# Kernel tuning notes

Hardware: AMD Instinct MI355X
Metric: run time of the kernel (lower is better)

The kernel has to match this reference:

```python
import jax, jax.numpy as jnp
import numpy as np

# Static part-graph structure (matches adj_matrix in init_kwargs; torch.nonzero row-major order)
ADJ = np.array([[0,1,0,0,0,0],
                [1,0,1,1,1,1],
                [0,1,0,0,0,0],
                [0,1,0,0,0,0],
                [0,1,0,0,0,0],
                [0,1,0,0,0,0]], dtype=np.int64)
_EDGES = np.argwhere(ADJ)            # [E,2] = (src, dst)
SRC = jnp.asarray(_EDGES[:, 0])
DST = jnp.asarray(_EDGES[:, 1])
NUM_PARTS = 6
# parts 1..4 are upper (use xh[0]), parts 5..6 lower (use xh[1])
HALVES = jnp.array([0, 0, 0, 0, 1, 1])


def setup_inputs() -> dict:
    key = jax.random.key(0)
    ks = jax.random.split(key, 12)
    B, H, W, Cin, h, P = 16, 96, 96, 256, 10, NUM_PARTS
    s = 0.05  # weight scale
    return {
        "p_fea":    jax.random.normal(ks[0], (B, Cin, H, W), jnp.float32),
        "xp_stack": jax.random.normal(ks[1], (P, B, h, H, W), jnp.float32),
        "xh_stack": jax.random.normal(ks[2], (2, B, h, H, W), jnp.float32),
        "w_att":  jax.random.normal(ks[3], (P, h), jnp.float32) * s,      # grouped 1x1 conv (groups=P)
        "b_att":  jnp.zeros((P,), jnp.float32),
        "w_dp_f": jax.random.normal(ks[4], (h, Cin), jnp.float32) * s,    # Part_Dependency: p_fea branch
        "w_dp_x": jax.random.normal(ks[5], (h, h), jnp.float32) * s,      # Part_Dependency: xp branch
        "b_dp":   jnp.zeros((h,), jnp.float32),
        "w_proj": jax.random.normal(ks[6], (P, h, Cin), jnp.float32) * s, # Decomposition proj (per part)
        "b_proj": jnp.zeros((P, h), jnp.float32),
        "w_gate": jax.random.normal(ks[7], (P, 2 * h), jnp.float32) * s,  # Decomposition gate on cat(xh,xp)
        "b_gate": jnp.zeros((P,), jnp.float32),
        "w_upd":  jax.random.normal(ks[8], (P, h, 3 * h), jnp.float32) * s,  # att_Update on cat(xp,xpp,xhp)
        "b_upd":  jnp.zeros((P, h), jnp.float32),
    }


def reference(p_fea, xp_stack, xh_stack, w_att, b_att, w_dp_f, w_dp_x, b_dp,
              w_proj, b_proj, w_gate, b_gate, w_upd, b_upd):
    # xp_stack: [P,B,h,H,W], p_fea: [B,Cin,H,W]
    P = xp_stack.shape[0]

    # grouped 1x1 conv + sigmoid -> per-part attention map [P,B,1,H,W]
    att = jax.nn.sigmoid(jnp.einsum('pbchw,pc->pbhw', xp_stack, w_att)
                         + b_att[:, None, None, None])[:, :, None]

    # Part_Dependency: dp_i = relu(W_f @ p_fea + W_x @ xp_i + b), shared weights -> [P,B,h,H,W]
    dp = jax.nn.relu(jnp.einsum('bchw,dc->bdhw', p_fea, w_dp_f)[None]
                     + jnp.einsum('pbchw,dc->pbdhw', xp_stack, w_dp_x)
                     + b_dp[None, None, :, None, None])

    # Pair_Part_Dependency per edge: sigmoid-gated fusion, then sum-aggregate at dst
    msg = att[SRC] * att[DST] * (dp[SRC] + xp_stack[DST])   # [E,B,h,H,W]
    xpp = jax.ops.segment_sum(msg, DST, num_segments=P)     # [P,B,h,H,W]

    # Decomposition: gate half-body feature onto a projection of p_fea (per-part weights)
    xh_sel = xh_stack[HALVES]                                # [P,B,h,H,W]
    proj = jnp.einsum('bchw,pdc->pbdhw', p_fea, w_proj) + b_proj[:, None, :, None, None]
    gate = jax.nn.sigmoid(jnp.einsum('pbchw,pc->pbhw',
                                     jnp.concatenate([xh_sel, xp_stack], axis=2), w_gate)
                          + b_gate[:, None, None, None])[:, :, None]
    xhp = gate * proj                                        # [P,B,h,H,W]

    # att_Update: residual update from cat(xp, xpp, xhp) via per-part 1x1 conv
    cat3 = jnp.concatenate([xp_stack, xpp, xhp], axis=2)     # [P,B,3h,H,W]
    xp_out = xp_stack + jax.nn.relu(jnp.einsum('pbchw,pdc->pbdhw', cat3, w_upd)
                                    + b_upd[:, None, :, None, None])
    return xp_out, xpp, xhp
```

## Files before the change

### kernel.cpp

```cpp
#include <hip/hip_runtime.h>

#define HWSZ 9216
#define CIN  256
#define NPER 8847360
#define PSTRIDE 1474560
#define IMG_STRIDE 2359296
#define BHW 92160

#define OFF_WATT  18432
#define OFF_BATT  18492
#define OFF_WDPX  18498
#define OFF_BDP   18598
#define OFF_BPROJ 18608
#define OFF_WGATE 18668
#define OFF_BGATE 18788
#define OFF_WUPD  18794
#define OFF_BUPD  20594
#define WS_TOTAL  20654
#define A_OFF_U16 41472
#define A_ELEMS   20480

typedef __attribute__((ext_vector_type(8))) short short8;
typedef __attribute__((ext_vector_type(4))) float f32x4;
typedef __attribute__((ext_vector_type(2))) float f32x2;

#define SS     66
#define L_S    0
#define L_DP1  4620
#define L_S1   5280
#define L_SA   5940
#define L_ATT  6008
#define L_GATE 6392
#define L_TOT  6776

static __device__ __forceinline__ unsigned short f2b(float f) {
  union { float f; unsigned int i; } v; v.f = f;
  unsigned int u = v.i;
  return (unsigned short)((u + 0x7fffu + ((u >> 16) & 1u)) >> 16);
}
static __device__ __forceinline__ float sigmoidf_(float x) {
  return 1.0f / (1.0f + __expf(-x));
}

__global__ void prep_weights(const float* __restrict__ w_att,
                             const float* __restrict__ b_att,
                             const float* __restrict__ w_dp_f,
                             const float* __restrict__ w_dp_x,
                             const float* __restrict__ b_dp,
                             const float* __restrict__ w_proj,
                             const float* __restrict__ b_proj,
                             const float* __restrict__ w_gate,
                             const float* __restrict__ b_gate,
                             const float* __restrict__ w_upd,
                             const float* __restrict__ b_upd,
                             float* __restrict__ ws)
{
  int i = blockIdx.x * 256 + threadIdx.x;
  if (i < A_ELEMS) {
    int j     = i & 7;
    int lane  = (i >> 3) & 63;
    int kstep = (i >> 9) & 7;
    int mtile = i >> 12;
    int m = mtile * 16 + (lane & 15);
    int k = kstep * 32 + ((lane >> 4) & 3) * 8 + j;
    float wv = (m < 10) ? w_dp_f[m * CIN + k]
             : (m < 70) ? w_proj[(m - 10) * CIN + k] : 0.f;
    ((unsigned short*)ws)[A_OFF_U16 + i] = f2b(wv);
  }
  if (i >= WS_TOTAL || i < OFF_WATT) return;
  float v;
  if      (i < OFF_BATT)  v = w_att [i - OFF_WATT ];
  else if (i < OFF_WDPX)  v = b_att [i - OFF_BATT ];
  else if (i < OFF_BDP)   v = w_dp_x[i - OFF_WDPX ];
  else if (i < OFF_BPROJ) v = b_dp  [i - OFF_BDP  ];
  else if (i < OFF_WGATE) v = b_proj[i - OFF_BPROJ];
  else if (i < OFF_BGATE) v = w_gate[i - OFF_WGATE];
  else if (i < OFF_WUPD)  v = b_gate[i - OFF_BGATE];
  else if (i < OFF_BUPD)  v = w_upd [i - OFF_WUPD ];
  else                    v = b_upd [i - OFF_BUPD ];
  ws[i] = v;
}

__global__ __launch_bounds__(256) void part_graph_main(
    const float* __restrict__ p_fea,
    const float* __restrict__ xp,
    const float* __restrict__ xh,
    const float* __restrict__ ws,
    float* __restrict__ out)
{
  __shared__ __align__(16) float smem[L_TOT];

  const int tid = threadIdx.x;
  const int b   = blockIdx.x / 144;
  const int s0  = (blockIdx.x % 144) * 64;

  for (int i = tid; i < 726; i += 256) smem[L_S1 + i] = 0.f;

  const int lane = tid & 63, wv = tid >> 6;
  const int l15  = lane & 15, quad = lane >> 4;
  const float* pf = p_fea + (size_t)b * IMG_STRIDE + s0 + wv * 16 + l15
                  + (size_t)quad * 8 * HWSZ;
  const short8* ap = (const short8*)((const unsigned short*)ws + A_OFF_U16);

  f32x4 acc[5];
#pragma unroll
  for (int mt = 0; mt < 5; ++mt) acc[mt] = (f32x4){0.f, 0.f, 0.f, 0.f};

  float t[2][8];
#pragma unroll
  for (int j = 0; j < 8; ++j) t[0][j] = pf[(size_t)j * HWSZ];
#pragma unroll
  for (int ks = 0; ks < 8; ++ks) {
    if (ks < 7) {
#pragma unroll
      for (int j = 0; j < 8; ++j)
        t[(ks + 1) & 1][j] = pf[(size_t)((ks + 1) * 32 + j) * HWSZ];
    }
    short8 bf;
#pragma unroll
    for (int j = 0; j < 8; ++j) bf[j] = (short)f2b(t[ks & 1][j]);
#pragma unroll
    for (int mt = 0; mt < 5; ++mt)
      acc[mt] = __builtin_amdgcn_mfma_f32_16x16x32_bf16(
          ap[(mt * 8 + ks) * 64 + lane], bf, acc[mt], 0, 0, 0);
  }

#pragma unroll
  for (int mt = 0; mt < 5; ++mt) {
#pragma unroll
    for (int r = 0; r < 4; ++r) {
      int m = mt * 16 + quad * 4 + r;
      if (m < 70) smem[L_S + m * SS + wv * 16 + l15] = acc[mt][r];
    }
  }

  __builtin_amdgcn_sched_barrier(0);

  const int ep = tid >> 5;
  const int px = (tid & 31) * 2;
  const size_t ebase = (size_t)b * BHW + s0 + px;

  f32x2 xp2[10];
  f32x2 att2, gate2;
  if (tid < 192) {
    const float* xpb = xp + (size_t)ep * PSTRIDE + ebase;
    const float* xhb = xh + (size_t)(ep >= 4 ? 1 : 0) * PSTRIDE + ebase;
    float ba = ws[OFF_BATT + ep], bg = ws[OFF_BGATE + ep];
    f32x2 asum = {ba, ba}, gsum = {bg, bg};
#pragma unroll
    for (int ch = 0; ch < 10; ++ch)
      xp2[ch] = *(const f32x2*)(xpb + (size_t)ch * HWSZ);
#pragma unroll
    for (int ch = 0; ch < 10; ++ch) {
      f32x2 hv = *(const f32x2*)(xhb + (size_t)ch * HWSZ);
      float wa  = ws[OFF_WATT  + ep * 10 + ch];
      float wgx = ws[OFF_WGATE + ep * 20 + 10 + ch];
      float wgh = ws[OFF_WGATE + ep * 20 + ch];
      asum.x = fmaf(wa,  xp2[ch].x, asum.x); asum.y = fmaf(wa,  xp2[ch].y, asum.y);
      gsum.x = fmaf(wgx, xp2[ch].x, gsum.x); gsum.y = fmaf(wgx, xp2[ch].y, gsum.y);
      gsum.x = fmaf(wgh, hv.x,      gsum.x); gsum.y = fmaf(wgh, hv.y,      gsum.y);
    }
    att2.x  = sigmoidf_(asum.x); att2.y  = sigmoidf_(asum.y);
    gate2.x = sigmoidf_(gsum.x); gate2.y = sigmoidf_(gsum.y);
    *(f32x2*)&smem[L_ATT  + ep * 64 + px] = att2;
    *(f32x2*)&smem[L_GATE + ep * 64 + px] = gate2;
  }
  __syncthreads();

  if (tid < 192) {
    if (ep == 1) {
#pragma unroll
      for (int ch = 0; ch < 10; ++ch) {
        f32x2 t2 = *(const f32x2*)&smem[L_S + ch * SS + px];
        float bd = ws[OFF_BDP + ch];
        t2.x += bd; t2.y += bd;
#pragma unroll
        for (int j = 0; j < 10; ++j) {
          float w = ws[OFF_WDPX + ch * 10 + j];
          t2.x = fmaf(w, xp2[j].x, t2.x); t2.y = fmaf(w, xp2[j].y, t2.y);
        }
        t2.x = fmaxf(t2.x, 0.f); t2.y = fmaxf(t2.y, 0.f);
        *(f32x2*)&smem[L_DP1 + ch * SS + px] = t2;
      }
    } else {
#pragma unroll
      for (int ch = 0; ch < 10; ++ch) {
        f32x2 t2 = *(const f32x2*)&smem[L_S + ch * SS + px];
        float bd = ws[OFF_BDP + ch];
        t2.x += bd; t2.y += bd;
#pragma unroll
        for (int j = 0; j < 10; ++j) {
          float w = ws[OFF_WDPX + ch * 10 + j];
          t2.x = fmaf(w, xp2[j].x, t2.x); t2.y = fmaf(w, xp2[j].y, t2.y);
        }
        t2.x = fmaxf(t2.x, 0.f); t2.y = fmaxf(t2.y, 0.f);
        atomicAdd(&smem[L_S1 + ch * SS + px],     att2.x * t2.x);
        atomicAdd(&smem[L_S1 + ch * SS + px + 1], att2.y * t2.y);
      }
      atomicAdd(&smem[L_SA + px],     att2.x);
      atomicAdd(&smem[L_SA + px + 1], att2.y);
    }
  }
  __syncthreads();

  if (tid < 192) {
    f32x2 att1 = *(const f32x2*)&smem[L_ATT + 64 + px];
    f32x2 aa = {0.f, 0.f}, sa2 = {0.f, 0.f};
    if (ep == 1) {
      sa2 = *(const f32x2*)&smem[L_SA + px];
    } else {
      aa.x = att1.x * att2.x; aa.y = att1.y * att2.y;
    }

    float* o0 = out + (size_t)ep * PSTRIDE + ebase;
    const float* wu = ws + OFF_WUPD + ep * 300;

    f32x2 u[10];
#pragma unroll
    for (int q = 0; q < 10; ++q) {
      float bu = ws[OFF_BUPD + ep * 10 + q];
      u[q].x = bu; u[q].y = bu;
    }

#pragma unroll
    for (int ch = 0; ch < 10; ++ch) {
      f32x2 xpp;
      if (ep == 1) {
        f32x2 s1v = *(const f32x2*)&smem[L_S1 + ch * SS + px];
        xpp.x = att1.x * fmaf(sa2.x, xp2[ch].x, s1v.x);
        xpp.y = att1.y * fmaf(sa2.y, xp2[ch].y, s1v.y);
      } else {
        f32x2 d1 = *(const f32x2*)&smem[L_DP1 + ch * SS + px];
        xpp.x = aa.x * (d1.x + xp2[ch].x);
        xpp.y = aa.y * (d1.y + xp2[ch].y);
      }
      f32x2 pr = *(const f32x2*)&smem[L_S + (10 + ep * 10 + ch) * SS + px];
      float bp = ws[OFF_BPROJ + ep * 10 + ch];
      f32x2 xhp;
      xhp.x = gate2.x * (pr.x + bp); xhp.y = gate2.y * (pr.y + bp);

      *(f32x2*)(o0 + (size_t)ch * HWSZ + NPER)             = xpp;
      *(f32x2*)(o0 + (size_t)ch * HWSZ + 2 * (size_t)NPER) = xhp;

#pragma unroll
      for (int q = 0; q < 10; ++q) {
        float w0 = wu[q * 30 + ch];
        float w1 = wu[q * 30 + 10 + ch];
        float w2 = wu[q * 30 + 20 + ch];
        u[q].x = fmaf(w0, xp2[ch].x, u[q].x); u[q].y = fmaf(w0, xp2[ch].y, u[q].y);
        u[q].x = fmaf(w1, xpp.x,     u[q].x); u[q].y = fmaf(w1, xpp.y,     u[q].y);
        u[q].x = fmaf(w2, xhp.x,     u[q].x); u[q].y = fmaf(w2, xhp.y,     u[q].y);
      }
    }
#pragma unroll
    for (int q = 0; q < 10; ++q) {
      f32x2 r;
      r.x = xp2[q].x + fmaxf(u[q].x, 0.f);
      r.y = xp2[q].y + fmaxf(u[q].y, 0.f);
      *(f32x2*)(o0 + (size_t)q * HWSZ) = r;
    }
  }
}

extern "C" void kernel_launch(void* const* d_in, const int* in_sizes, int n_in,
                              void* d_out, int out_size, void* d_ws, size_t ws_size,
                              hipStream_t stream) {
  const float* p_fea = (const float*)d_in[0];
  const float* xp    = (const float*)d_in[1];
  const float* xh    = (const float*)d_in[2];
  float* ws = (float*)d_ws;

  prep_weights<<<(WS_TOTAL + 255) / 256, 256, 0, stream>>>(
      (const float*)d_in[3],  (const float*)d_in[4],
      (const float*)d_in[5],  (const float*)d_in[6],
      (const float*)d_in[7],  (const float*)d_in[8],
      (const float*)d_in[9],  (const float*)d_in[10],
      (const float*)d_in[11], (const float*)d_in[12],
      (const float*)d_in[13], ws);

  part_graph_main<<<2304, 256, 0, stream>>>(
      p_fea, xp, xh, ws, (float*)d_out);
}
```

Measured before the change: 394.8 us.

## Map one part per wavefront with scalar per-part weights, replacing two-pixel threads

The epilogue now gives each wavefront one part, with one pixel per lane, and waves 0-1 also handle parts 4-5. Previously 192 of the 256 threads each did two pixels and one wave sat idle. Because each part index is wave-uniform, readfirstlane makes the per-part weight loads scalar, which should cut VGPR use and vector weight traffic. The trade-off is narrower scalar float loads instead of f32x2 vector loads, and waves 0-1 carry twice the work of waves 2-3, which may leave the load unbalanced.

```diff
diff --git a/kernel.cpp b/kernel.cpp
--- a/kernel.cpp
+++ b/kernel.cpp
@@ -22,7 +22,6 @@
 
 typedef __attribute__((ext_vector_type(8))) short short8;
 typedef __attribute__((ext_vector_type(4))) float f32x4;
-typedef __attribute__((ext_vector_type(2))) float f32x2;
 
 #define SS     66
 #define L_S    0
@@ -81,6 +80,93 @@
   ws[i] = v;
 }
 
+
+static __device__ __forceinline__ void prefetch_ag(
+    int p, int px, size_t ebase,
+    const float* __restrict__ xp, const float* __restrict__ xh,
+    const float* __restrict__ ws, float* __restrict__ smem,
+    float* __restrict__ xpv, float& att)
+{
+  const int pu = __builtin_amdgcn_readfirstlane(p);
+  const float* xpb = xp + (size_t)pu * PSTRIDE + ebase;
+  const float* xhb = xh + (size_t)(pu >= 4 ? 1 : 0) * PSTRIDE + ebase;
+  float asum = ws[OFF_BATT + pu], gsum = ws[OFF_BGATE + pu];
+#pragma unroll
+  for (int ch = 0; ch < 10; ++ch)
+    xpv[ch] = xpb[(size_t)ch * HWSZ];
+#pragma unroll
+  for (int ch = 0; ch < 10; ++ch) {
+    float hv = xhb[(size_t)ch * HWSZ];
+    asum = fmaf(ws[OFF_WATT  + pu * 10 + ch],      xpv[ch], asum);
+    gsum = fmaf(ws[OFF_WGATE + pu * 20 + 10 + ch], xpv[ch], gsum);
+    gsum = fmaf(ws[OFF_WGATE + pu * 20 + ch],      hv,      gsum);
+  }
+  att = sigmoidf_(asum);
+  smem[L_ATT  + pu * 64 + px] = att;
+  smem[L_GATE + pu * 64 + px] = sigmoidf_(gsum);
+}
+
+static __device__ __forceinline__ void e1_body(
+    int p, int px, const float* __restrict__ ws,
+    float* __restrict__ smem, const float* __restrict__ xpv, float att)
+{
+#pragma unroll
+  for (int ch = 0; ch < 10; ++ch) {
+    float tv = smem[L_S + ch * SS + px] + ws[OFF_BDP + ch];
+#pragma unroll
+    for (int j = 0; j < 10; ++j)
+      tv = fmaf(ws[OFF_WDPX + ch * 10 + j], xpv[j], tv);
+    tv = fmaxf(tv, 0.f);
+    if (p == 1) smem[L_DP1 + ch * SS + px] = tv;
+    else        atomicAdd(&smem[L_S1 + ch * SS + px], att * tv);
+  }
+  if (p != 1) atomicAdd(&smem[L_SA + px], att);
+}
+
+static __device__ __forceinline__ void e2_body(
+    int p, int px, size_t ebase, const float* __restrict__ ws,
+    const float* __restrict__ smem, const float* __restrict__ xpv,
+    float* __restrict__ out)
+{
+  const int pu = __builtin_amdgcn_readfirstlane(p);
+  float attp = smem[L_ATT + pu * 64 + px];
+  float att1 = smem[L_ATT + 64 + px];
+  float g    = smem[L_GATE + pu * 64 + px];
+  float aa   = att1 * attp;
+  float sa   = smem[L_SA + px];
+
+  float* o0 = out + (size_t)pu * PSTRIDE + ebase;
+  const float* wu = ws + OFF_WUPD + pu * 300;
+
+  float u[10];
+#pragma unroll
+  for (int q = 0; q < 10; ++q) u[q] = ws[OFF_BUPD + pu * 10 + q];
+
+#pragma unroll
+  for (int ch = 0; ch < 10; ++ch) {
+    float xpp;
+    if (pu == 1)
+      xpp = att1 * fmaf(sa, xpv[ch], smem[L_S1 + ch * SS + px]);
+    else
+      xpp = aa * (smem[L_DP1 + ch * SS + px] + xpv[ch]);
+    float pr  = smem[L_S + (10 + pu * 10 + ch) * SS + px];
+    float xhp = g * (pr + ws[OFF_BPROJ + pu * 10 + ch]);
+
+    o0[(size_t)ch * HWSZ + NPER]             = xpp;
+    o0[(size_t)ch * HWSZ + 2 * (size_t)NPER] = xhp;
+
+#pragma unroll
+    for (int q = 0; q < 10; ++q) {
+      u[q] = fmaf(wu[q * 30 + ch],      xpv[ch], u[q]);
+      u[q] = fmaf(wu[q * 30 + 10 + ch], xpp,     u[q]);
+      u[q] = fmaf(wu[q * 30 + 20 + ch], xhp,     u[q]);
+    }
+  }
+#pragma unroll
+  for (int q = 0; q < 10; ++q)
+    o0[(size_t)q * HWSZ] = xpv[q] + fmaxf(u[q], 0.f);
+}
+
 __global__ __launch_bounds__(256) void part_graph_main(
     const float* __restrict__ p_fea,
     const float* __restrict__ xp,
@@ -136,130 +222,24 @@
 
   __builtin_amdgcn_sched_barrier(0);
 
-  const int ep = tid >> 5;
-  const int px = (tid & 31) * 2;
+  const int px = lane;
   const size_t ebase = (size_t)b * BHW + s0 + px;
 
-  f32x2 xp2[10];
-  f32x2 att2, gate2;
-  if (tid < 192) {
-    const float* xpb = xp + (size_t)ep * PSTRIDE + ebase;
-    const float* xhb = xh + (size_t)(ep >= 4 ? 1 : 0) * PSTRIDE + ebase;
-    float ba = ws[OFF_BATT + ep], bg = ws[OFF_BGATE + ep];
-    f32x2 asum = {ba, ba}, gsum = {bg, bg};
-#pragma unroll
-    for (int ch = 0; ch < 10; ++ch)
-      xp2[ch] = *(const f32x2*)(xpb + (size_t)ch * HWSZ);
-#pragma unroll
-    for (int ch = 0; ch < 10; ++ch) {
-      f32x2 hv = *(const f32x2*)(xhb + (size_t)ch * HWSZ);
-      float wa  = ws[OFF_WATT  + ep * 10 + ch];
-      float wgx = ws[OFF_WGATE + ep * 20 + 10 + ch];
-      float wgh = ws[OFF_WGATE + ep * 20 + ch];
-      asum.x = fmaf(wa,  xp2[ch].x, asum.x); asum.y = fmaf(wa,  xp2[ch].y, asum.y);
-      gsum.x = fmaf(wgx, xp2[ch].x, gsum.x); gsum.y = fmaf(wgx, xp2[ch].y, gsum.y);
-      gsum.x = fmaf(wgh, hv.x,      gsum.x); gsum.y = fmaf(wgh, hv.y,      gsum.y);
-    }
-    att2.x  = sigmoidf_(asum.x); att2.y  = sigmoidf_(asum.y);
-    gate2.x = sigmoidf_(gsum.x); gate2.y = sigmoidf_(gsum.y);
-    *(f32x2*)&smem[L_ATT  + ep * 64 + px] = att2;
-    *(f32x2*)&smem[L_GATE + ep * 64 + px] = gate2;
-  }
+  float xpv[10], att2;
+  float xpvB[10], attB;
+  prefetch_ag(wv, px, ebase, xp, xh, ws, smem, xpv, att2);
+  if (wv < 2)
+    prefetch_ag(4 + wv, px, ebase, xp, xh, ws, smem, xpvB, attB);
   __syncthreads();
 
-  if (tid < 192) {
-    if (ep == 1) {
-#pragma unroll
-      for (int ch = 0; ch < 10; ++ch) {
-        f32x2 t2 = *(const f32x2*)&smem[L_S + ch * SS + px];
-        float bd = ws[OFF_BDP + ch];
-        t2.x += bd; t2.y += bd;
-#pragma unroll
-        for (int j = 0; j < 10; ++j) {
-          float w = ws[OFF_WDPX + ch * 10 + j];
-          t2.x = fmaf(w, xp2[j].x, t2.x); t2.y = fmaf(w, xp2[j].y, t2.y);
-        }
-        t2.x = fmaxf(t2.x, 0.f); t2.y = fmaxf(t2.y, 0.f);
-        *(f32x2*)&smem[L_DP1 + ch * SS + px] = t2;
-      }
-    } else {
-#pragma unroll
-      for (int ch = 0; ch < 10; ++ch) {
-        f32x2 t2 = *(const f32x2*)&smem[L_S + ch * SS + px];
-        float bd = ws[OFF_BDP + ch];
-        t2.x += bd; t2.y += bd;
-#pragma unroll
-        for (int j = 0; j < 10; ++j) {
-          float w = ws[OFF_WDPX + ch * 10 + j];
-          t2.x = fmaf(w, xp2[j].x, t2.x); t2.y = fmaf(w, xp2[j].y, t2.y);
-        }
-        t2.x = fmaxf(t2.x, 0.f); t2.y = fmaxf(t2.y, 0.f);
-        atomicAdd(&smem[L_S1 + ch * SS + px],     att2.x * t2.x);
-        atomicAdd(&smem[L_S1 + ch * SS + px + 1], att2.y * t2.y);
-      }
-      atomicAdd(&smem[L_SA + px],     att2.x);
-      atomicAdd(&smem[L_SA + px + 1], att2.y);
-    }
-  }
+  e1_body(wv, px, ws, smem, xpv, att2);
+  if (wv < 2)
+    e1_body(4 + wv, px, ws, smem, xpvB, attB);
   __syncthreads();
 
-  if (tid < 192) {
-    f32x2 att1 = *(const f32x2*)&smem[L_ATT + 64 + px];
-    f32x2 aa = {0.f, 0.f}, sa2 = {0.f, 0.f};
-    if (ep == 1) {
-      sa2 = *(const f32x2*)&smem[L_SA + px];
-    } else {
-      aa.x = att1.x * att2.x; aa.y = att1.y * att2.y;
-    }
-
-    float* o0 = out + (size_t)ep * PSTRIDE + ebase;
-    const float* wu = ws + OFF_WUPD + ep * 300;
-
-    f32x2 u[10];
-#pragma unroll
-    for (int q = 0; q < 10; ++q) {
-      float bu = ws[OFF_BUPD + ep * 10 + q];
-      u[q].x = bu; u[q].y = bu;
-    }
-
-#pragma unroll
-    for (int ch = 0; ch < 10; ++ch) {
-      f32x2 xpp;
-      if (ep == 1) {
-        f32x2 s1v = *(const f32x2*)&smem[L_S1 + ch * SS + px];
-        xpp.x = att1.x * fmaf(sa2.x, xp2[ch].x, s1v.x);
-        xpp.y = att1.y * fmaf(sa2.y, xp2[ch].y, s1v.y);
-      } else {
-        f32x2 d1 = *(const f32x2*)&smem[L_DP1 + ch * SS + px];
-        xpp.x = aa.x * (d1.x + xp2[ch].x);
-        xpp.y = aa.y * (d1.y + xp2[ch].y);
-      }
-      f32x2 pr = *(const f32x2*)&smem[L_S + (10 + ep * 10 + ch) * SS + px];
-      float bp = ws[OFF_BPROJ + ep * 10 + ch];
-      f32x2 xhp;
-      xhp.x = gate2.x * (pr.x + bp); xhp.y = gate2.y * (pr.y + bp);
-
-      *(f32x2*)(o0 + (size_t)ch * HWSZ + NPER)             = xpp;
-      *(f32x2*)(o0 + (size_t)ch * HWSZ + 2 * (size_t)NPER) = xhp;
-
-#pragma unroll
-      for (int q = 0; q < 10; ++q) {
-        float w0 = wu[q * 30 + ch];
-        float w1 = wu[q * 30 + 10 + ch];
-        float w2 = wu[q * 30 + 20 + ch];
-        u[q].x = fmaf(w0, xp2[ch].x, u[q].x); u[q].y = fmaf(w0, xp2[ch].y, u[q].y);
-        u[q].x = fmaf(w1, xpp.x,     u[q].x); u[q].y = fmaf(w1, xpp.y,     u[q].y);
-        u[q].x = fmaf(w2, xhp.x,     u[q].x); u[q].y = fmaf(w2, xhp.y,     u[q].y);
-      }
-    }
-#pragma unroll
-    for (int q = 0; q < 10; ++q) {
-      f32x2 r;
-      r.x = xp2[q].x + fmaxf(u[q].x, 0.f);
-      r.y = xp2[q].y + fmaxf(u[q].y, 0.f);
-      *(f32x2*)(o0 + (size_t)q * HWSZ) = r;
-    }
-  }
+  e2_body(wv, px, ebase, ws, smem, xpv, out);
+  if (wv < 2)
+    e2_body(4 + wv, px, ebase, ws, smem, xpvB, out);
 }
 
 extern "C" void kernel_launch(void* const* d_in, const int* in_sizes, int n_in,
```

Result: faster. 337.0 us (-14.6%).
